# Kernel tuning notes

Hardware: AMD Instinct MI355X
Metric: run time of the kernel (lower is better)

Reference implementation:

```python
import jax, jax.numpy as jnp
import numpy as np

V_REST = 0.0
V_RESET = 0.0
V_TH = 1.27
TAU = 50.0
SPIKE_DURATION = 1
SCALE = 100.0  # SurrGradSpike.scale


@jax.custom_vjp
def spike(x):
    return (x > 0).astype(x.dtype)

def _spike_fwd(x):
    return (x > 0).astype(x.dtype), x

def _spike_bwd(x, g):
    # normalized negative part of fast sigmoid (Zenke & Ganguli 2018)
    return (g / (SCALE * jnp.abs(x) + 1.0) ** 2,)

spike.defvjp(_spike_fwd, _spike_bwd)


def _shift(a, k):
    # a[:, j] -> a[:, j + k], zero padded out of range
    if k == 0:
        return a
    if k > 0:
        return jnp.pad(a[:, k:], ((0, 0), (0, k)))
    return jnp.pad(a[:, :k], ((0, 0), (-k, 0)))


def _lif(ode, decay):
    ode2 = ode[..., 0]          # [B, T]
    B, T = ode2.shape
    ode_t = ode2.T              # [T, B] for scan

    def step(carry, inp):
        v, counter, z = carry   # z = remaining steps whose dv reads are zeroed
        t, x = inp
        v = v - decay * (v - V_REST)
        v = jnp.where(counter == 1, V_RESET, v)
        # dv[:, t] was zeroed by a spike within the previous 5 steps (torch in-place window)
        x_eff = jnp.where(z > 0, 0.0, x)
        v = v + x_eff
        v = jnp.where(counter > 1, V_TH, v)
        s = spike(v - V_TH)
        s_d = jax.lax.stop_gradient(s)
        counter = counter + (SPIKE_DURATION + 1) * s_d
        v = jnp.where(counter > 1, V_TH, v)
        # spike at t zeroes dv[:, t-1:t+6]; at t==0 the torch slice [-1:6] is empty
        z = jnp.where((s_d > 0) & (t >= 1), 5.0, jnp.maximum(z - 1.0, 0.0))
        counter = jnp.maximum(counter - 1.0, 0.0)
        return (v, counter, z), (v, s, s_d)

    v0 = jnp.full((B,), V_REST, dtype=ode2.dtype)
    c0 = jnp.zeros((B,), dtype=ode2.dtype)
    z0 = jnp.zeros((B,), dtype=ode2.dtype)
    ts = jnp.arange(T)
    _, (v_rec, s_rec, sd_rec) = jax.lax.scan(step, (v0, c0, z0), (ts, ode_t))
    v_rec = v_rec.T             # [B, T]
    s_rec = s_rec.T             # [B, T]

    sp = sd_rec.T > 0           # detached spike mask [B, T]
    sp = sp.at[:, 0].set(False)  # spike at t=0 zeroes nothing (empty slice in torch)
    # column j of dv is zeroed iff a spike occurred at t' in [j-5, j+1]
    zero_mask = jnp.zeros_like(sp)
    for k in range(-5, 2):
        zero_mask = zero_mask | _shift(sp, k)
    dv = jnp.where(zero_mask, 0.0, ode2)
    return v_rec, s_rec, dv


def setup_inputs() -> dict:
    key = jax.random.key(0)
    B, T = 2048, 4096
    ode = jax.random.normal(key, (B, T, 1), dtype=jnp.float32)
    decay = jnp.float32(1.0 / TAU)  # LIF.decay parameter (learn_tau=False)
    return {"ode": ode, "decay": decay}


def reference(ode, decay):
    return _lif(ode, decay)
```

## Files before the change

### kernel.cpp

```cpp
#include <hip/hip_runtime.h>

constexpr int   T   = 4096;
constexpr float VTH = 1.27f;
constexpr int   K   = 32;
constexpr int   L   = T / K;
constexpr int   LG  = L / 4;
constexpr int   WG  = 160;

__device__ __forceinline__ bool sstep(float x, float decay, float& v, unsigned& h, bool& gate) {
    float t1 = __fmul_rn(decay, v);
    float vd = __fsub_rn(v, t1);
    float xe = gate ? 0.0f : x;
    float vn = __fadd_rn(vd, xe);
    bool  s  = vn > VTH;
    v = s ? 0.0f : vn;
    bool g4 = (h & 15u) != 0u;
    h = (h << 1) | (s ? 1u : 0u);
    gate = s || g4;
    return s;
}

__device__ __forceinline__ bool ostep(float x, float decay, float& v, unsigned& h, bool& gate,
                                      float& vo, float& so, float& dvo, float xprev) {
    float t1 = __fmul_rn(decay, v);
    float vd = __fsub_rn(v, t1);
    float xe = gate ? 0.0f : x;
    float vn = __fadd_rn(vd, xe);
    bool  s  = vn > VTH;
    vo = s ? VTH  : vn;
    so = s ? 1.0f : 0.0f;
    v  = s ? 0.0f : vn;
    bool z6 = s || ((h & 63u) != 0u);
    dvo = z6 ? 0.0f : xprev;
    bool g4 = (h & 15u) != 0u;
    h = (h << 1) | (s ? 1u : 0u);
    gate = s || g4;
    return s;
}

__device__ __forceinline__ void ogroup(float4 X, float decay, float& v, unsigned& h, bool& gate,
                                       float& xprev, float4& vo, float4& so,
                                       float& close, float& px, float& py, float& pz) {
    ostep(X.x, decay, v, h, gate, vo.x, so.x, close, xprev); xprev = X.x;
    ostep(X.y, decay, v, h, gate, vo.y, so.y, px,    xprev); xprev = X.y;
    ostep(X.z, decay, v, h, gate, vo.z, so.z, py,    xprev); xprev = X.z;
    ostep(X.w, decay, v, h, gate, vo.w, so.w, pz,    xprev); xprev = X.w;
}

__global__ __launch_bounds__(64, 1)
void lif_spec(const float* __restrict__ ode, const float* __restrict__ decay_p,
              float* __restrict__ vout, float* __restrict__ sout, float* __restrict__ dvout,
              float2* __restrict__ Sst, float2* __restrict__ Est, int B) {
    __shared__ float4 tv[64 * 5];
    __shared__ float4 ts[64 * 5];
    __shared__ float4 td[2][64 * 5];

    const int tid = threadIdx.x;
    const int gg  = blockIdx.x * 64;
    const int rb  = gg % B;
    const int k   = gg / B;
    const int b   = rb + tid;
    const float decay = decay_p[0];

    const size_t bt = (size_t)b * T;
    const float4* __restrict__ x4 = (const float4*)(ode + bt);

    const int g0f = k * LG;
    const int wg  = (k == 0) ? 0 : (k * LG < WG ? k * LG : WG);
    float v = 0.0f; unsigned h = 0u; bool gate = false;
    float xprev = 0.0f;

    if (wg > 0) {
        const float4* __restrict__ xw = x4 + (g0f - wg);
        const bool t0row = (g0f - wg == 0);
        float4 Q[16];
#pragma unroll
        for (int i = 0; i < 16; ++i) Q[i] = xw[i];
        for (int c = 0; c < wg; c += 16) {
#pragma unroll
            for (int i = 0; i < 16; ++i) {
                if (i == 0 && c == 0 && t0row) {
                    sstep(Q[0].x, decay, v, h, gate); h = 0u; gate = false;
                    sstep(Q[0].y, decay, v, h, gate);
                    sstep(Q[0].z, decay, v, h, gate);
                    sstep(Q[0].w, decay, v, h, gate);
                } else {
                    sstep(Q[i].x, decay, v, h, gate);
                    sstep(Q[i].y, decay, v, h, gate);
                    sstep(Q[i].z, decay, v, h, gate);
                    sstep(Q[i].w, decay, v, h, gate);
                }
                Q[i] = xw[c + i + 16];
            }
        }
        Sst[k * B + b] = make_float2(v, __uint_as_float(h & 127u));
    }

    int rowoff0 = (rb + (tid >> 2)) * T + k * L + (tid & 3) * 4;
    const int wbase = tid * 5;
    const int rbase = (tid >> 2) * 5 + (tid & 3);

    float xla = (k < K - 1) ? ode[bt + (size_t)(k + 1) * L] : 0.0f;
    float4 A0 = x4[g0f],     A1 = x4[g0f + 1], A2 = x4[g0f + 2], A3 = x4[g0f + 3];
    float4 B0 = x4[g0f + 4], B1 = x4[g0f + 5], B2 = x4[g0f + 6], B3 = x4[g0f + 7];
    float4 Pd;

#define OG(X, gidx) { float4 V_, S_; float cl_, p0_, p1_, p2_; \
        ogroup(X, decay, v, h, gate, xprev, V_, S_, cl_, p0_, p1_, p2_); \
        if ((gidx) > 0) { Pd.w = cl_; td[(((gidx)-1) >> 2) & 1][wbase + (((gidx)-1) & 3)] = Pd; } \
        Pd.x = p0_; Pd.y = p1_; Pd.z = p2_; \
        tv[wbase + ((gidx) & 3)] = V_; ts[wbase + ((gidx) & 3)] = S_; }

#define FLUSH(q) { __syncthreads(); \
        float4 Vv0 = tv[rbase], Vv1 = tv[rbase + 80], Vv2 = tv[rbase + 160], Vv3 = tv[rbase + 240]; \
        float4 Ss0 = ts[rbase], Ss1 = ts[rbase + 80], Ss2 = ts[rbase + 160], Ss3 = ts[rbase + 240]; \
        *(float4*)(vout + rowoff0 + (q)*16)            = Vv0; \
        *(float4*)(vout + rowoff0 + 16*T + (q)*16)     = Vv1; \
        *(float4*)(vout + rowoff0 + 32*T + (q)*16)     = Vv2; \
        *(float4*)(vout + rowoff0 + 48*T + (q)*16)     = Vv3; \
        *(float4*)(sout + rowoff0 + (q)*16)            = Ss0; \
        *(float4*)(sout + rowoff0 + 16*T + (q)*16)     = Ss1; \
        *(float4*)(sout + rowoff0 + 32*T + (q)*16)     = Ss2; \
        *(float4*)(sout + rowoff0 + 48*T + (q)*16)     = Ss3; \
        if ((q) >= 1) { \
            float4 Dd0 = td[((q)-1)&1][rbase],       Dd1 = td[((q)-1)&1][rbase + 80]; \
            float4 Dd2 = td[((q)-1)&1][rbase + 160], Dd3 = td[((q)-1)&1][rbase + 240]; \
            *(float4*)(dvout + rowoff0 + ((q)-1)*16)        = Dd0; \
            *(float4*)(dvout + rowoff0 + 16*T + ((q)-1)*16) = Dd1; \
            *(float4*)(dvout + rowoff0 + 32*T + ((q)-1)*16) = Dd2; \
            *(float4*)(dvout + rowoff0 + 48*T + ((q)-1)*16) = Dd3; } }

    {
        if (k == 0) {
            float4 V_, S_; float dvd;
            bool s0 = ostep(A0.x, decay, v, h, gate, V_.x, S_.x, dvd, xprev); xprev = A0.x;
            h = 0u; gate = false;
            bool s1 = ostep(A0.y, decay, v, h, gate, V_.y, S_.y, Pd.x, xprev); xprev = A0.y;
            ostep(A0.z, decay, v, h, gate, V_.z, S_.z, Pd.y, xprev); xprev = A0.z;
            ostep(A0.w, decay, v, h, gate, V_.w, S_.w, Pd.z, xprev); xprev = A0.w;
            if (s0 && s1) V_.z = VTH;
            tv[wbase] = V_; ts[wbase] = S_;
        } else {
            float4 V_, S_; float cl_;
            ogroup(A0, decay, v, h, gate, xprev, V_, S_, cl_, Pd.x, Pd.y, Pd.z);
            tv[wbase] = V_; ts[wbase] = S_;
        }
        A0 = x4[g0f + 8];
        OG(A1, 1) A1 = x4[g0f + 9];
        OG(A2, 2) A2 = x4[g0f + 10];
        OG(A3, 3) A3 = x4[g0f + 11];
        FLUSH(0)
    }

#define MQ(q, Xs) \
        OG(Xs##0, 4*(q)+0) Xs##0 = x4[g0f + (4*(q)+8  < LG ? 4*(q)+8  : LG-1)]; \
        OG(Xs##1, 4*(q)+1) Xs##1 = x4[g0f + (4*(q)+9  < LG ? 4*(q)+9  : LG-1)]; \
        OG(Xs##2, 4*(q)+2) Xs##2 = x4[g0f + (4*(q)+10 < LG ? 4*(q)+10 : LG-1)]; \
        OG(Xs##3, 4*(q)+3) Xs##3 = x4[g0f + (4*(q)+11 < LG ? 4*(q)+11 : LG-1)]; \
        FLUSH(q)
    MQ(1, B) MQ(2, A) MQ(3, B) MQ(4, A) MQ(5, B) MQ(6, A) MQ(7, B)
#undef MQ
#undef OG

    Est[k * B + b] = make_float2(v, __uint_as_float(h & 127u));

    if (k < K - 1) {
        float vo_, so_;
        ostep(xla, decay, v, h, gate, vo_, so_, Pd.w, xprev);
    } else {
        Pd.w = ((h & 63u) != 0u) ? 0.0f : xprev;
    }
    td[1][wbase + 3] = Pd;
    __syncthreads();
    {
        float4 Dd0 = td[1][rbase],       Dd1 = td[1][rbase + 80];
        float4 Dd2 = td[1][rbase + 160], Dd3 = td[1][rbase + 240];
        *(float4*)(dvout + rowoff0 + 7*16)        = Dd0;
        *(float4*)(dvout + rowoff0 + 16*T + 7*16) = Dd1;
        *(float4*)(dvout + rowoff0 + 32*T + 7*16) = Dd2;
        *(float4*)(dvout + rowoff0 + 48*T + 7*16) = Dd3;
    }
#undef FLUSH
}

__global__ __launch_bounds__(64, 1)
void lif_fix(const float* __restrict__ ode, const float* __restrict__ decay_p,
             float* __restrict__ vout, float* __restrict__ sout, float* __restrict__ dvout,
             const float2* __restrict__ Sst, const float2* __restrict__ Est, int B) {
    const int b = blockIdx.x * 64 + threadIdx.x;
    const float decay = decay_p[0];

    float2 E  = Est[b];
    float2 S1 = Sst[B + b];
    float2 E1 = Est[B + b];
    for (int k = 1; k < K; ++k) {
        float2 S = S1, Ek = E1;
        if (k + 1 < K) { S1 = Sst[(k + 1) * B + b]; E1 = Est[(k + 1) * B + b]; }
        bool match = (S.x == E.x) && (__float_as_uint(S.y) == __float_as_uint(E.y));
        if (match) { E = Ek; continue; }

        const size_t bt = (size_t)b * T;
        const float4* __restrict__ x4 = (const float4*)(ode + bt);
        float4* __restrict__ v4 = (float4*)(vout + bt);
        float4* __restrict__ s4 = (float4*)(sout + bt);
        float4* __restrict__ d4 = (float4*)(dvout + bt);
        const int g0f = k * LG;

        float v = E.x; unsigned h = __float_as_uint(E.y);
        bool gate = (h & 31u) != 0u;
        float xprev = 0.0f;
        float4 pend;

        float4 Q0 = x4[g0f], Q1 = x4[g0f + 1], Q2 = x4[g0f + 2], Q3 = x4[g0f + 3];
        {
            float4 vo, so; float cl;
            ogroup(Q0, decay, v, h, gate, xprev, vo, so, cl, pend.x, pend.y, pend.z);
            v4[g0f] = vo; s4[g0f] = so;
            Q0 = x4[g0f + 4];
        }
#define FPROC(cc, Q) { float4 vo, so; float px, py, pz; \
            ogroup(Q, decay, v, h, gate, xprev, vo, so, pend.w, px, py, pz); \
            d4[g0f + (cc) - 1] = pend; \
            pend.x = px; pend.y = py; pend.z = pz; \
            v4[g0f + (cc)] = vo; s4[g0f + (cc)] = so; }
        FPROC(1, Q1) Q1 = x4[g0f + 5];
        FPROC(2, Q2) Q2 = x4[g0f + 6];
        FPROC(3, Q3) Q3 = x4[g0f + 7];
        for (int c0 = 4; c0 < LG; c0 += 4) {
            FPROC(c0,     Q0) Q0 = x4[g0f + (c0 + 4 < LG ? c0 + 4 : LG - 1)];
            FPROC(c0 + 1, Q1) Q1 = x4[g0f + (c0 + 5 < LG ? c0 + 5 : LG - 1)];
            FPROC(c0 + 2, Q2) Q2 = x4[g0f + (c0 + 6 < LG ? c0 + 6 : LG - 1)];
            FPROC(c0 + 3, Q3) Q3 = x4[g0f + (c0 + 7 < LG ? c0 + 7 : LG - 1)];
        }
#undef FPROC
        E = make_float2(v, __uint_as_float(h & 127u));
        if (k < K - 1) {
            float xla = ode[bt + (size_t)(k + 1) * L];
            float vo_, so_;
            ostep(xla, decay, v, h, gate, vo_, so_, pend.w, xprev);
        } else {
            pend.w = ((h & 63u) != 0u) ? 0.0f : xprev;
        }
        d4[g0f + LG - 1] = pend;
    }
}

extern "C" void kernel_launch(void* const* d_in, const int* in_sizes, int n_in,
                              void* d_out, int out_size, void* d_ws, size_t ws_size,
                              hipStream_t stream) {
    const float* ode   = (const float*)d_in[0];
    const float* decay = (const float*)d_in[1];
    float* out = (float*)d_out;

    const int BT = in_sizes[0];
    const int B  = BT / T;

    float* vout  = out;
    float* sout  = out + (size_t)BT;
    float* dvout = out + 2 * (size_t)BT;

    float2* Sst = (float2*)d_ws;
    float2* Est = Sst + (size_t)K * B;

    lif_spec<<<dim3((B * K) / 64), dim3(64), 0, stream>>>(ode, decay, vout, sout, dvout,
                                                          Sst, Est, B);
    lif_fix<<<dim3(B / 64), dim3(64), 0, stream>>>(ode, decay, vout, sout, dvout,
                                                   Sst, Est, B);
}
```

Measured before the change: 180.1 us.

## Pre-transpose input into interleaved layout and flush outputs in wider swizzled tiles

```diff
diff --git a/kernel.cpp b/kernel.cpp
--- a/kernel.cpp
+++ b/kernel.cpp
@@ -47,13 +47,54 @@
     ostep(X.w, decay, v, h, gate, vo.w, so.w, pz,    xprev); xprev = X.w;
 }
 
+__global__ __launch_bounds__(256)
+void xt_pass(const float* __restrict__ ode, float4* __restrict__ xT, int B) {
+    __shared__ float4 tile[64][8];
+    const int tid = threadIdx.x;
+    const int ntt = T / 32;
+    const int tt  = blockIdx.x % ntt;
+    const int rb  = (blockIdx.x / ntt) * 64;
+    const int g0  = tt * 8;
+    const float4* __restrict__ x4g = (const float4*)ode;
+
+    {
+        int r = tid >> 3, c = tid & 7;
+        tile[r][c ^ (r & 7)]           = x4g[(size_t)(rb + r)      * (T / 4) + g0 + c];
+        int r2 = r + 32;
+        tile[r2][c ^ (r2 & 7)]         = x4g[(size_t)(rb + r2)     * (T / 4) + g0 + c];
+    }
+    __syncthreads();
+    {
+        int l = tid & 63, j = tid >> 6;
+        size_t obase = ((size_t)(rb >> 6) * (T / 4) + g0) * 64;
+        xT[obase + (size_t)j       * 64 + l] = tile[l][j       ^ (l & 7)];
+        xT[obase + (size_t)(j + 4) * 64 + l] = tile[l][(j + 4) ^ (l & 7)];
+    }
+}
+
+__device__ __forceinline__ void flush_pair(int p, int tid, int rb, int k,
+        float* __restrict__ vout, float* __restrict__ sout, float* __restrict__ dvout,
+        const float4 (*tv)[8], const float4 (*ts)[8], const float4 (*td)[64][8]) {
+    __syncthreads();
+    const int cc = (tid & 7) ^ (tid >> 3);
+#pragma unroll
+    for (int jj = 0; jj < 8; ++jj) {
+        int rr = jj * 8 + (tid >> 3);
+        size_t off = (size_t)(rb + rr) * T + k * L + p * 32 + (tid & 7) * 4;
+        *(float4*)(vout + off) = tv[rr][cc];
+        *(float4*)(sout + off) = ts[rr][cc];
+        if (p >= 1) *(float4*)(dvout + off - 32) = td[(p - 1) & 1][rr][cc];
+    }
+    __syncthreads();
+}
+
 __global__ __launch_bounds__(64, 1)
-void lif_spec(const float* __restrict__ ode, const float* __restrict__ decay_p,
+void lif_spec(const float4* __restrict__ xT, const float* __restrict__ decay_p,
               float* __restrict__ vout, float* __restrict__ sout, float* __restrict__ dvout,
               float2* __restrict__ Sst, float2* __restrict__ Est, int B) {
-    __shared__ float4 tv[64 * 5];
-    __shared__ float4 ts[64 * 5];
-    __shared__ float4 td[2][64 * 5];
+    __shared__ float4 tv[64][8];
+    __shared__ float4 ts[64][8];
+    __shared__ float4 td[2][64][8];
 
     const int tid = threadIdx.x;
     const int gg  = blockIdx.x * 64;
@@ -61,9 +102,10 @@
     const int k   = gg / B;
     const int b   = rb + tid;
     const float decay = decay_p[0];
-
-    const size_t bt = (size_t)b * T;
-    const float4* __restrict__ x4 = (const float4*)(ode + bt);
+    const int xs7 = tid & 7;
+
+    const size_t xb = (size_t)(rb >> 6) * (T / 4) * 64 + tid;
+#define XLD(g) xT[xb + (size_t)(g) * 64]
 
     const int g0f = k * LG;
     const int wg  = (k == 0) ? 0 : (k * LG < WG ? k * LG : WG);
@@ -71,11 +113,11 @@
     float xprev = 0.0f;
 
     if (wg > 0) {
-        const float4* __restrict__ xw = x4 + (g0f - wg);
+        const size_t xwb = xb + (size_t)(g0f - wg) * 64;
         const bool t0row = (g0f - wg == 0);
         float4 Q[16];
 #pragma unroll
-        for (int i = 0; i < 16; ++i) Q[i] = xw[i];
+        for (int i = 0; i < 16; ++i) Q[i] = xT[xwb + (size_t)i * 64];
         for (int c = 0; c < wg; c += 16) {
 #pragma unroll
             for (int i = 0; i < 16; ++i) {
@@ -90,45 +132,22 @@
                     sstep(Q[i].z, decay, v, h, gate);
                     sstep(Q[i].w, decay, v, h, gate);
                 }
-                Q[i] = xw[c + i + 16];
+                Q[i] = xT[xwb + (size_t)(c + i + 16) * 64];
             }
         }
         Sst[k * B + b] = make_float2(v, __uint_as_float(h & 127u));
     }
 
-    int rowoff0 = (rb + (tid >> 2)) * T + k * L + (tid & 3) * 4;
-    const int wbase = tid * 5;
-    const int rbase = (tid >> 2) * 5 + (tid & 3);
-
-    float xla = (k < K - 1) ? ode[bt + (size_t)(k + 1) * L] : 0.0f;
-    float4 A0 = x4[g0f],     A1 = x4[g0f + 1], A2 = x4[g0f + 2], A3 = x4[g0f + 3];
-    float4 B0 = x4[g0f + 4], B1 = x4[g0f + 5], B2 = x4[g0f + 6], B3 = x4[g0f + 7];
+    float4 A0 = XLD(g0f),     A1 = XLD(g0f + 1), A2 = XLD(g0f + 2), A3 = XLD(g0f + 3);
+    float4 B0 = XLD(g0f + 4), B1 = XLD(g0f + 5), B2 = XLD(g0f + 6), B3 = XLD(g0f + 7);
     float4 Pd;
 
 #define OG(X, gidx) { float4 V_, S_; float cl_, p0_, p1_, p2_; \
         ogroup(X, decay, v, h, gate, xprev, V_, S_, cl_, p0_, p1_, p2_); \
-        if ((gidx) > 0) { Pd.w = cl_; td[(((gidx)-1) >> 2) & 1][wbase + (((gidx)-1) & 3)] = Pd; } \
+        if ((gidx) > 0) { Pd.w = cl_; \
+            td[(((gidx) - 1) >> 3) & 1][tid][(((gidx) - 1) & 7) ^ xs7] = Pd; } \
         Pd.x = p0_; Pd.y = p1_; Pd.z = p2_; \
-        tv[wbase + ((gidx) & 3)] = V_; ts[wbase + ((gidx) & 3)] = S_; }
-
-#define FLUSH(q) { __syncthreads(); \
-        float4 Vv0 = tv[rbase], Vv1 = tv[rbase + 80], Vv2 = tv[rbase + 160], Vv3 = tv[rbase + 240]; \
-        float4 Ss0 = ts[rbase], Ss1 = ts[rbase + 80], Ss2 = ts[rbase + 160], Ss3 = ts[rbase + 240]; \
-        *(float4*)(vout + rowoff0 + (q)*16)            = Vv0; \
-        *(float4*)(vout + rowoff0 + 16*T + (q)*16)     = Vv1; \
-        *(float4*)(vout + rowoff0 + 32*T + (q)*16)     = Vv2; \
-        *(float4*)(vout + rowoff0 + 48*T + (q)*16)     = Vv3; \
-        *(float4*)(sout + rowoff0 + (q)*16)            = Ss0; \
-        *(float4*)(sout + rowoff0 + 16*T + (q)*16)     = Ss1; \
-        *(float4*)(sout + rowoff0 + 32*T + (q)*16)     = Ss2; \
-        *(float4*)(sout + rowoff0 + 48*T + (q)*16)     = Ss3; \
-        if ((q) >= 1) { \
-            float4 Dd0 = td[((q)-1)&1][rbase],       Dd1 = td[((q)-1)&1][rbase + 80]; \
-            float4 Dd2 = td[((q)-1)&1][rbase + 160], Dd3 = td[((q)-1)&1][rbase + 240]; \
-            *(float4*)(dvout + rowoff0 + ((q)-1)*16)        = Dd0; \
-            *(float4*)(dvout + rowoff0 + 16*T + ((q)-1)*16) = Dd1; \
-            *(float4*)(dvout + rowoff0 + 32*T + ((q)-1)*16) = Dd2; \
-            *(float4*)(dvout + rowoff0 + 48*T + ((q)-1)*16) = Dd3; } }
+        tv[tid][((gidx) & 7) ^ xs7] = V_; ts[tid][((gidx) & 7) ^ xs7] = S_; }
 
     {
         if (k == 0) {
@@ -139,48 +158,58 @@
             ostep(A0.z, decay, v, h, gate, V_.z, S_.z, Pd.y, xprev); xprev = A0.z;
             ostep(A0.w, decay, v, h, gate, V_.w, S_.w, Pd.z, xprev); xprev = A0.w;
             if (s0 && s1) V_.z = VTH;
-            tv[wbase] = V_; ts[wbase] = S_;
+            tv[tid][xs7] = V_; ts[tid][xs7] = S_;
         } else {
             float4 V_, S_; float cl_;
             ogroup(A0, decay, v, h, gate, xprev, V_, S_, cl_, Pd.x, Pd.y, Pd.z);
-            tv[wbase] = V_; ts[wbase] = S_;
-        }
-        A0 = x4[g0f + 8];
-        OG(A1, 1) A1 = x4[g0f + 9];
-        OG(A2, 2) A2 = x4[g0f + 10];
-        OG(A3, 3) A3 = x4[g0f + 11];
-        FLUSH(0)
-    }
-
-#define MQ(q, Xs) \
-        OG(Xs##0, 4*(q)+0) Xs##0 = x4[g0f + (4*(q)+8  < LG ? 4*(q)+8  : LG-1)]; \
-        OG(Xs##1, 4*(q)+1) Xs##1 = x4[g0f + (4*(q)+9  < LG ? 4*(q)+9  : LG-1)]; \
-        OG(Xs##2, 4*(q)+2) Xs##2 = x4[g0f + (4*(q)+10 < LG ? 4*(q)+10 : LG-1)]; \
-        OG(Xs##3, 4*(q)+3) Xs##3 = x4[g0f + (4*(q)+11 < LG ? 4*(q)+11 : LG-1)]; \
-        FLUSH(q)
-    MQ(1, B) MQ(2, A) MQ(3, B) MQ(4, A) MQ(5, B) MQ(6, A) MQ(7, B)
-#undef MQ
+            tv[tid][xs7] = V_; ts[tid][xs7] = S_;
+        }
+        A0 = XLD(g0f + 8);
+        OG(A1, 1) A1 = XLD(g0f + 9);
+        OG(A2, 2) A2 = XLD(g0f + 10);
+        OG(A3, 3) A3 = XLD(g0f + 11);
+        OG(B0, 4) B0 = XLD(g0f + 12);
+        OG(B1, 5) B1 = XLD(g0f + 13);
+        OG(B2, 6) B2 = XLD(g0f + 14);
+        OG(B3, 7) B3 = XLD(g0f + 15);
+        flush_pair(0, tid, rb, k, vout, sout, dvout, tv, ts, td);
+    }
+    OG(A0, 8)  A0 = XLD(g0f + 16); OG(A1, 9)  A1 = XLD(g0f + 17);
+    OG(A2, 10) A2 = XLD(g0f + 18); OG(A3, 11) A3 = XLD(g0f + 19);
+    OG(B0, 12) B0 = XLD(g0f + 20); OG(B1, 13) B1 = XLD(g0f + 21);
+    OG(B2, 14) B2 = XLD(g0f + 22); OG(B3, 15) B3 = XLD(g0f + 23);
+    flush_pair(1, tid, rb, k, vout, sout, dvout, tv, ts, td);
+    OG(A0, 16) A0 = XLD(g0f + 24); OG(A1, 17) A1 = XLD(g0f + 25);
+    OG(A2, 18) A2 = XLD(g0f + 26); OG(A3, 19) A3 = XLD(g0f + 27);
+    OG(B0, 20) B0 = XLD(g0f + 28); OG(B1, 21) B1 = XLD(g0f + 29);
+    OG(B2, 22) B2 = XLD(g0f + 30); OG(B3, 23) B3 = XLD(g0f + 31);
+    flush_pair(2, tid, rb, k, vout, sout, dvout, tv, ts, td);
+    OG(A0, 24) OG(A1, 25) OG(A2, 26) OG(A3, 27)
+    OG(B0, 28) OG(B1, 29) OG(B2, 30) OG(B3, 31)
+    flush_pair(3, tid, rb, k, vout, sout, dvout, tv, ts, td);
 #undef OG
 
     Est[k * B + b] = make_float2(v, __uint_as_float(h & 127u));
 
     if (k < K - 1) {
+        float xla = XLD((k + 1) * LG).x;
         float vo_, so_;
         ostep(xla, decay, v, h, gate, vo_, so_, Pd.w, xprev);
     } else {
         Pd.w = ((h & 63u) != 0u) ? 0.0f : xprev;
     }
-    td[1][wbase + 3] = Pd;
+    td[1][tid][7 ^ xs7] = Pd;
     __syncthreads();
     {
-        float4 Dd0 = td[1][rbase],       Dd1 = td[1][rbase + 80];
-        float4 Dd2 = td[1][rbase + 160], Dd3 = td[1][rbase + 240];
-        *(float4*)(dvout + rowoff0 + 7*16)        = Dd0;
-        *(float4*)(dvout + rowoff0 + 16*T + 7*16) = Dd1;
-        *(float4*)(dvout + rowoff0 + 32*T + 7*16) = Dd2;
-        *(float4*)(dvout + rowoff0 + 48*T + 7*16) = Dd3;
-    }
-#undef FLUSH
+        const int cc = (tid & 7) ^ (tid >> 3);
+#pragma unroll
+        for (int jj = 0; jj < 8; ++jj) {
+            int rr = jj * 8 + (tid >> 3);
+            size_t off = (size_t)(rb + rr) * T + k * L + 3 * 32 + (tid & 7) * 4;
+            *(float4*)(dvout + off) = td[1][rr][cc];
+        }
+    }
+#undef XLD
 }
 
 __global__ __launch_bounds__(64, 1)
@@ -261,8 +290,10 @@
 
     float2* Sst = (float2*)d_ws;
     float2* Est = Sst + (size_t)K * B;
-
-    lif_spec<<<dim3((B * K) / 64), dim3(64), 0, stream>>>(ode, decay, vout, sout, dvout,
+    float4* xT  = (float4*)((char*)d_ws + 2 * (size_t)K * B * sizeof(float2));
+
+    xt_pass<<<dim3((T / 32) * (B / 64)), dim3(256), 0, stream>>>(ode, xT, B);
+    lif_spec<<<dim3((B * K) / 64), dim3(64), 0, stream>>>(xT, decay, vout, sout, dvout,
                                                           Sst, Est, B);
     lif_fix<<<dim3(B / 64), dim3(64), 0, stream>>>(ode, decay, vout, sout, dvout,
                                                    Sst, Est, B);
```

New measurement: 184.2 us. 2.3% more time.
